# Kernel tuning notes

Hardware: AMD Instinct MI355X
Metric: run time of the kernel (lower is better)

## Reference

```python
import jax, jax.numpy as jnp
import numpy as np

N_NODES = 50000
N_EDGES = 800000
IN_DIM = 128
HID = 32
HEADS = 4
OUT_DIM = 64
NEG_SLOPE = 0.2  # DGL GATConv default


def setup_inputs() -> dict:
    key = jax.random.key(0)
    ks = jax.random.split(key, 20)

    def glorot(k, shape):
        fan = shape[0] + shape[-1]
        return (jax.random.normal(k, shape, jnp.float32) * np.sqrt(2.0 / fan)).astype(jnp.float32)

    inp = {
        "h": jax.random.normal(ks[0], (N_NODES, IN_DIM), jnp.float32),
        "src": jax.random.randint(ks[1], (N_EDGES,), 0, N_NODES, jnp.int32),
        "dst": jax.random.randint(ks[2], (N_EDGES,), 0, N_NODES, jnp.int32),
        # layer 0: in_dim -> hidden, HEADS heads, relu
        "W1": glorot(ks[3], (IN_DIM, HEADS * HID)),
        "al1": glorot(ks[4], (HEADS, HID)),
        "ar1": glorot(ks[5], (HEADS, HID)),
        "b1": jnp.zeros((HEADS * HID,), jnp.float32),
        # layer 1 (hidden): hidden*heads -> hidden, HEADS heads, relu
        "W2": glorot(ks[6], (HEADS * HID, HEADS * HID)),
        "al2": glorot(ks[7], (HEADS, HID)),
        "ar2": glorot(ks[8], (HEADS, HID)),
        "b2": jnp.zeros((HEADS * HID,), jnp.float32),
        # layer 2 (output): hidden*heads -> out_dim, 1 head, no activation
        "W3": glorot(ks[9], (HEADS * HID, OUT_DIM)),
        "al3": glorot(ks[10], (1, OUT_DIM)),
        "ar3": glorot(ks[11], (1, OUT_DIM)),
        "b3": jnp.zeros((OUT_DIM,), jnp.float32),
    }
    return inp


def gat_conv(h, src, dst, W, attn_l, attn_r, bias, heads, out_dim, use_relu):
    n = h.shape[0]
    feat = (h @ W).reshape(n, heads, out_dim)              # [N,H,D]
    el = jnp.sum(feat * attn_l[None], axis=-1)             # [N,H]
    er = jnp.sum(feat * attn_r[None], axis=-1)             # [N,H]
    e = jax.nn.leaky_relu(el[src] + er[dst], NEG_SLOPE)    # [E,H] per-edge logits
    # segment softmax over incoming edges of each dst node
    emax = jax.ops.segment_max(e, dst, num_segments=n)     # [N,H] (-inf for isolated nodes, never gathered)
    ee = jnp.exp(e - emax[dst])                            # [E,H]
    denom = jax.ops.segment_sum(ee, dst, num_segments=n)   # [N,H]
    alpha = ee / denom[dst]                                # [E,H]
    msg = feat[src] * alpha[:, :, None]                    # [E,H,D] gather + weight
    out = jax.ops.segment_sum(msg, dst, num_segments=n)    # [N,H,D] scatter-add
    out = out + bias.reshape(1, heads, out_dim)
    if use_relu:
        out = jax.nn.relu(out)
    return out.reshape(n, heads * out_dim)


def reference(h, src, dst, W1, al1, ar1, b1, W2, al2, ar2, b2, W3, al3, ar3, b3):
    # dropout is identity in eval mode
    h1 = gat_conv(h, src, dst, W1, al1, ar1, b1, HEADS, HID, True)
    h2 = gat_conv(h1, src, dst, W2, al2, ar2, b2, HEADS, HID, True)
    h3 = gat_conv(h2, src, dst, W3, al3, ar3, b3, 1, OUT_DIM, False)
    return h3
```

## Files before the change

kernel.cpp:

```cpp
#include <hip/hip_runtime.h>
#include <hip/hip_fp16.h>

#define NNODES 50000
#define NEDGES 800000
#define HISTB 256

__device__ __forceinline__ float leaky(float x) { return x >= 0.f ? x : 0.2f * x; }

typedef _Float16 f16x8 __attribute__((ext_vector_type(8)));
typedef float f32x4 __attribute__((ext_vector_type(4)));

struct __align__(8)  half4v { __half2 h0, h1; };
struct __align__(16) half8v { __half2 h0, h1, h2, h3; };

template<int F, int H, bool FP16IN, bool DO_HIST>
__global__ __launch_bounds__(256) void gemm_mfma_k(const void* __restrict__ Xv,
                                                   const float* __restrict__ W,
                                                   const float* __restrict__ al,
                                                   const float* __restrict__ ar,
                                                   __half* __restrict__ Yh,
                                                   float* __restrict__ el,
                                                   float* __restrict__ er, int n,
                                                   int nGemm,
                                                   const int* __restrict__ dst,
                                                   int* __restrict__ cnt,
                                                   int* __restrict__ rank) {
    constexpr int K = 128;
    constexpr int ROWS = 64;
    constexpr int LDK = K + 8;
    constexpr int NT = F / 16;

    if (DO_HIST && blockIdx.x >= nGemm) {
        int b = blockIdx.x - nGemm;
        for (int e = b * 256 + threadIdx.x; e < NEDGES; e += HISTB * 256)
            rank[e] = atomicAdd(&cnt[dst[e]], 1);
        return;
    }

    __shared__ __align__(16) __half Xs[ROWS * LDK];
    __shared__ __align__(16) __half Wt[F * LDK];

    const int tid = threadIdx.x;
    const int r0 = blockIdx.x * ROWS;

    if constexpr (FP16IN) {
        const __half* X = (const __half*)Xv;
        for (int i = tid; i < ROWS * (K / 8); i += 256) {
            int r = i >> 4, c8 = i & 15;
            int row = r0 + r;
            half8v v;
            __half2 z = __halves2half2(__float2half_rn(0.f), __float2half_rn(0.f));
            v.h0 = z; v.h1 = z; v.h2 = z; v.h3 = z;
            if (row < n) v = ((const half8v*)X)[(size_t)row * (K / 8) + c8];
            *(half8v*)&Xs[r * LDK + c8 * 8] = v;
        }
    } else {
        const float* X = (const float*)Xv;
        for (int i = tid; i < ROWS * (K / 4); i += 256) {
            int r = i >> 5, c4 = i & 31;
            int row = r0 + r;
            float4 v = (row < n) ? ((const float4*)X)[(size_t)row * (K / 4) + c4]
                                 : make_float4(0.f, 0.f, 0.f, 0.f);
            __half* d = &Xs[r * LDK + c4 * 4];
            d[0] = __float2half_rn(v.x); d[1] = __float2half_rn(v.y);
            d[2] = __float2half_rn(v.z); d[3] = __float2half_rn(v.w);
        }
    }
    for (int i = tid; i < K * (F / 4); i += 256) {
        int k = i / (F / 4), n4 = i % (F / 4);
        float4 v = ((const float4*)W)[i];
        int nn = n4 * 4;
        Wt[(nn + 0) * LDK + k] = __float2half_rn(v.x);
        Wt[(nn + 1) * LDK + k] = __float2half_rn(v.y);
        Wt[(nn + 2) * LDK + k] = __float2half_rn(v.z);
        Wt[(nn + 3) * LDK + k] = __float2half_rn(v.w);
    }
    __syncthreads();

    const int wv = tid >> 6, lane = tid & 63;
    const int cl = lane & 15, kg = lane >> 4;

    f32x4 acc[NT];
    #pragma unroll
    for (int t = 0; t < NT; t++) acc[t] = (f32x4){0.f, 0.f, 0.f, 0.f};

    #pragma unroll
    for (int ks = 0; ks < K / 32; ks++) {
        f16x8 a = *(const f16x8*)&Xs[(16 * wv + cl) * LDK + ks * 32 + kg * 8];
        #pragma unroll
        for (int t = 0; t < NT; t++) {
            f16x8 b = *(const f16x8*)&Wt[(16 * t + cl) * LDK + ks * 32 + kg * 8];
            acc[t] = __builtin_amdgcn_mfma_f32_16x16x32_f16(a, b, acc[t], 0, 0, 0);
        }
    }

    #pragma unroll
    for (int t = 0; t < NT; t++)
        #pragma unroll
        for (int j = 0; j < 4; j++) {
            int row = r0 + 16 * wv + 4 * kg + j;
            if (row < n) Yh[(size_t)row * F + 16 * t + cl] = __float2half_rn(acc[t][j]);
        }

    float alv[NT], arv[NT];
    #pragma unroll
    for (int t = 0; t < NT; t++) { alv[t] = al[16 * t + cl]; arv[t] = ar[16 * t + cl]; }

    if (H == 1) {
        float pl[4], pr[4];
        #pragma unroll
        for (int j = 0; j < 4; j++) {
            pl[j] = 0.f; pr[j] = 0.f;
            #pragma unroll
            for (int t = 0; t < NT; t++) { pl[j] += acc[t][j] * alv[t]; pr[j] += acc[t][j] * arv[t]; }
        }
        #pragma unroll
        for (int off = 1; off < 16; off <<= 1)
            #pragma unroll
            for (int j = 0; j < 4; j++) { pl[j] += __shfl_xor(pl[j], off); pr[j] += __shfl_xor(pr[j], off); }
        if (cl == 0)
            #pragma unroll
            for (int j = 0; j < 4; j++) {
                int row = r0 + 16 * wv + 4 * kg + j;
                if (row < n) { el[row] = pl[j]; er[row] = pr[j]; }
            }
    } else {
        float pl[4][4], pr[4][4];
        #pragma unroll
        for (int hh = 0; hh < 4; hh++)
            #pragma unroll
            for (int j = 0; j < 4; j++) {
                pl[hh][j] = acc[2 * hh][j] * alv[2 * hh] + acc[2 * hh + 1][j] * alv[2 * hh + 1];
                pr[hh][j] = acc[2 * hh][j] * arv[2 * hh] + acc[2 * hh + 1][j] * arv[2 * hh + 1];
            }
        #pragma unroll
        for (int off = 1; off < 16; off <<= 1)
            #pragma unroll
            for (int hh = 0; hh < 4; hh++)
                #pragma unroll
                for (int j = 0; j < 4; j++) {
                    pl[hh][j] += __shfl_xor(pl[hh][j], off);
                    pr[hh][j] += __shfl_xor(pr[hh][j], off);
                }
        if (cl == 0)
            #pragma unroll
            for (int j = 0; j < 4; j++) {
                int row = r0 + 16 * wv + 4 * kg + j;
                if (row < n)
                    #pragma unroll
                    for (int hh = 0; hh < 4; hh++) {
                        el[row * 4 + hh] = pl[hh][j];
                        er[row * 4 + hh] = pr[hh][j];
                    }
            }
    }
}

__global__ void scan_blk_k(const int* __restrict__ cnt, int* __restrict__ offs,
                           int* __restrict__ bsum, int n) {
    __shared__ int sm[256];
    int tid = threadIdx.x;
    int i = blockIdx.x * 256 + tid;
    int v = (i < n) ? cnt[i] : 0;
    sm[tid] = v;
    __syncthreads();
    for (int off = 1; off < 256; off <<= 1) {
        int t = (tid >= off) ? sm[tid - off] : 0;
        __syncthreads();
        sm[tid] += t;
        __syncthreads();
    }
    if (i < n) offs[i] = sm[tid] - v;
    if (tid == 255) bsum[blockIdx.x] = sm[255];
}

__global__ void scan_addtop_k(int* __restrict__ offs, const int* __restrict__ bsum,
                              int n, int nb) {
    __shared__ int sm[256];
    int tid = threadIdx.x;
    int v = (tid < nb) ? bsum[tid] : 0;
    sm[tid] = v;
    __syncthreads();
    for (int off = 1; off < 256; off <<= 1) {
        int t = (tid >= off) ? sm[tid - off] : 0;
        __syncthreads();
        sm[tid] += t;
        __syncthreads();
    }
    int prefix = (blockIdx.x > 0) ? sm[blockIdx.x - 1] : 0;
    int i = blockIdx.x * 256 + tid;
    if (i < n) offs[i] += prefix;
    if (i == 0) offs[n] = NEDGES;
}

__global__ void scatter_k(const int* __restrict__ src, const int* __restrict__ dst,
                          const int* __restrict__ rank, const int* __restrict__ offs,
                          int* __restrict__ esrc) {
    int e = blockIdx.x * blockDim.x + threadIdx.x;
    if (e < NEDGES) esrc[offs[dst[e]] + rank[e]] = src[e];
}

__global__ __launch_bounds__(256) void node_agg4_k(const int* __restrict__ offs,
                                                   const int* __restrict__ esrc,
                                                   const float* __restrict__ el,
                                                   const float* __restrict__ er,
                                                   const __half* __restrict__ feat,
                                                   const float* __restrict__ bias,
                                                   __half* __restrict__ out) {
    const int lane = threadIdx.x & 63;
    const int gw0 = (blockIdx.x * 256 + threadIdx.x) >> 6;
    const int NW = (gridDim.x * 256) >> 6;

    const int h  = lane & 3;
    const int q  = lane >> 4;
    const int cl = lane & 15;
    const int hd = cl >> 2;

    float4 ba = *(const float4*)&bias[8 * cl];
    float4 bb = *(const float4*)&bias[8 * cl + 4];

    for (int wid = gw0; wid < NNODES; wid += NW) {
        int beg = offs[wid], end = offs[wid + 1];
        float erh = er[wid * 4 + h];

        float acc[8] = {0.f, 0.f, 0.f, 0.f, 0.f, 0.f, 0.f, 0.f};
        float dsum = 0.f;
        for (int base = beg; base < end; base += 16) {
            int rem = end - base;
            if (rem > 16) rem = 16;
            int sv = 0;
            if (lane < rem) sv = esrc[base + lane];
            int se = __shfl(sv, lane >> 2);
            float p = 0.f;
            if ((lane >> 2) < rem)
                p = __expf(leaky(el[se * 4 + h] + erh));
            dsum += p;
            #pragma unroll
            for (int e = 0; e < 16 && e < rem; e += 4) {
                int eidx = e + q;
                int s = __shfl(sv, eidx);
                float a = __shfl(p, eidx * 4 + hd);
                half8v hv = *(const half8v*)&feat[(size_t)s * 128 + 8 * cl];
                float2 f0 = __half22float2(hv.h0);
                float2 f1 = __half22float2(hv.h1);
                float2 f2 = __half22float2(hv.h2);
                float2 f3 = __half22float2(hv.h3);
                acc[0] += f0.x * a; acc[1] += f0.y * a;
                acc[2] += f1.x * a; acc[3] += f1.y * a;
                acc[4] += f2.x * a; acc[5] += f2.y * a;
                acc[6] += f3.x * a; acc[7] += f3.y * a;
            }
        }
        #pragma unroll
        for (int c = 0; c < 8; c++) {
            acc[c] += __shfl_xor(acc[c], 16);
            acc[c] += __shfl_xor(acc[c], 32);
        }
        #pragma unroll
        for (int off = 4; off < 64; off <<= 1) dsum += __shfl_xor(dsum, off);
        float dh = __shfl(dsum, hd);
        float inv = dh > 0.f ? 1.f / dh : 0.f;
        if (q == 0) {
            float v0 = fmaxf(acc[0] * inv + ba.x, 0.f), v1 = fmaxf(acc[1] * inv + ba.y, 0.f);
            float v2 = fmaxf(acc[2] * inv + ba.z, 0.f), v3 = fmaxf(acc[3] * inv + ba.w, 0.f);
            float v4 = fmaxf(acc[4] * inv + bb.x, 0.f), v5 = fmaxf(acc[5] * inv + bb.y, 0.f);
            float v6 = fmaxf(acc[6] * inv + bb.z, 0.f), v7 = fmaxf(acc[7] * inv + bb.w, 0.f);
            half8v hv;
            hv.h0 = __halves2half2(__float2half_rn(v0), __float2half_rn(v1));
            hv.h1 = __halves2half2(__float2half_rn(v2), __float2half_rn(v3));
            hv.h2 = __halves2half2(__float2half_rn(v4), __float2half_rn(v5));
            hv.h3 = __halves2half2(__float2half_rn(v6), __float2half_rn(v7));
            *(half8v*)&out[(size_t)wid * 128 + 8 * cl] = hv;
        }
    }
}

__global__ __launch_bounds__(256) void node_agg1_k(const int* __restrict__ offs,
                                                   const int* __restrict__ esrc,
                                                   const float* __restrict__ el,
                                                   const float* __restrict__ er,
                                                   const __half* __restrict__ feat,
                                                   const float* __restrict__ bias,
                                                   float* __restrict__ out) {
    const int lane = threadIdx.x & 63;
    const int gw0 = (blockIdx.x * 256 + threadIdx.x) >> 6;
    const int NW = (gridDim.x * 256) >> 6;

    const int q  = lane >> 4;
    const int cl = lane & 15;
    float4 b4 = *(const float4*)&bias[4 * cl];

    for (int wid = gw0; wid < NNODES; wid += NW) {
        int beg = offs[wid], end = offs[wid + 1];
        float erd = er[wid];

        float acc[4] = {0.f, 0.f, 0.f, 0.f};
        float dsum = 0.f;
        for (int base = beg; base < end; base += 64) {
            int rem = end - base;
            if (rem > 64) rem = 64;
            int sv = 0;
            float p = 0.f;
            if (lane < rem) {
                sv = esrc[base + lane];
                p = __expf(leaky(el[sv] + erd));
            }
            dsum += p;
            #pragma unroll 4
            for (int e = 0; e < rem; e += 4) {
                int eidx = e + q;
                int s = __shfl(sv, eidx);
                float a = __shfl(p, eidx);
                half4v hv = *(const half4v*)&feat[(size_t)s * 64 + 4 * cl];
                float2 f0 = __half22float2(hv.h0);
                float2 f1 = __half22float2(hv.h1);
                acc[0] += f0.x * a; acc[1] += f0.y * a;
                acc[2] += f1.x * a; acc[3] += f1.y * a;
            }
        }
        #pragma unroll
        for (int c = 0; c < 4; c++) {
            acc[c] += __shfl_xor(acc[c], 16);
            acc[c] += __shfl_xor(acc[c], 32);
        }
        #pragma unroll
        for (int off = 1; off < 64; off <<= 1) dsum += __shfl_xor(dsum, off);
        float inv = dsum > 0.f ? 1.f / dsum : 0.f;
        if (q == 0) {
            *(float4*)&out[(size_t)wid * 64 + 4 * cl] =
                make_float4(acc[0] * inv + b4.x, acc[1] * inv + b4.y,
                            acc[2] * inv + b4.z, acc[3] * inv + b4.w);
        }
    }
}

extern "C" void kernel_launch(void* const* d_in, const int* in_sizes, int n_in,
                              void* d_out, int out_size, void* d_ws, size_t ws_size,
                              hipStream_t stream) {
    const float* h   = (const float*)d_in[0];
    const int*   src = (const int*)d_in[1];
    const int*   dst = (const int*)d_in[2];
    const float* W1  = (const float*)d_in[3];
    const float* al1 = (const float*)d_in[4];
    const float* ar1 = (const float*)d_in[5];
    const float* b1  = (const float*)d_in[6];
    const float* W2  = (const float*)d_in[7];
    const float* al2 = (const float*)d_in[8];
    const float* ar2 = (const float*)d_in[9];
    const float* b2  = (const float*)d_in[10];
    const float* W3  = (const float*)d_in[11];
    const float* al3 = (const float*)d_in[12];
    const float* ar3 = (const float*)d_in[13];
    const float* b3  = (const float*)d_in[14];
    float* out = (float*)d_out;

    const int n = NNODES;
    __half* feat16 = (__half*)d_ws;
    __half* hbuf16 = feat16 + (size_t)n * 128;
    float*  el     = (float*)(hbuf16 + (size_t)n * 128);
    float*  er     = el + (size_t)n * 4;
    int*    cnt    = (int*)(er + (size_t)n * 4);
    int*    offs   = cnt + n;
    int*    esrc   = offs + (n + 1);
    int*    bsum   = esrc + NEDGES;
    int*    rank   = bsum + 256;

    const int gemmBlocks = (n + 63) / 64;
    const int nBlk = (n + 255) / 256;
    const int eBlk = (NEDGES + 255) / 256;
    const int aggBlk = 2048;

    hipMemsetAsync(cnt, 0, (size_t)n * sizeof(int), stream);

    gemm_mfma_k<128, 4, false, true><<<gemmBlocks + HISTB, 256, 0, stream>>>(
        h, W1, al1, ar1, feat16, el, er, n, gemmBlocks, dst, cnt, rank);

    scan_blk_k<<<nBlk, 256, 0, stream>>>(cnt, offs, bsum, n);
    scan_addtop_k<<<nBlk, 256, 0, stream>>>(offs, bsum, n, nBlk);
    scatter_k<<<eBlk, 256, 0, stream>>>(src, dst, rank, offs, esrc);

    node_agg4_k<<<aggBlk, 256, 0, stream>>>(offs, esrc, el, er, feat16, b1, hbuf16);

    gemm_mfma_k<128, 4, true, false><<<gemmBlocks, 256, 0, stream>>>(
        hbuf16, W2, al2, ar2, feat16, el, er, n, gemmBlocks, nullptr, nullptr, nullptr);
    node_agg4_k<<<aggBlk, 256, 0, stream>>>(offs, esrc, el, er, feat16, b2, hbuf16);

    gemm_mfma_k<64, 1, true, false><<<gemmBlocks, 256, 0, stream>>>(
        hbuf16, W3, al3, ar3, feat16, el, er, n, gemmBlocks, nullptr, nullptr, nullptr);
    node_agg1_k<<<aggBlk, 256, 0, stream>>>(offs, esrc, el, er, feat16, b3, out);
}
```

Before: 222.1 us.

## Pretranspose weights to fp16 once and load GEMM operands directly from global

A new small kernel converts and transposes all three weight matrices to fp16 once per call into workspace. The GEMM kernels drop their shared-memory staging of X and W and read MFMA operands straight from global memory. Each block no longer converts and transposes the full weight matrix into LDS, and the barrier goes away. The cost is one extra launch, plus weight reads that rely on L2/L1 caching and A-loads that may be less coalesced.

```diff
diff --git a/kernel.cpp b/kernel.cpp
--- a/kernel.cpp
+++ b/kernel.cpp
@@ -13,9 +13,26 @@
 struct __align__(8)  half4v { __half2 h0, h1; };
 struct __align__(16) half8v { __half2 h0, h1, h2, h3; };
 
+__global__ __launch_bounds__(256) void wtrans_k(const float* __restrict__ W1,
+                                                const float* __restrict__ W2,
+                                                const float* __restrict__ W3,
+                                                __half* __restrict__ Wt) {
+    int i = blockIdx.x * 256 + threadIdx.x;
+    if (i < 16384) {
+        int k = i >> 7, c = i & 127;
+        Wt[c * 128 + k] = __float2half_rn(W1[i]);
+    } else if (i < 32768) {
+        int e = i - 16384, k = e >> 7, c = e & 127;
+        Wt[16384 + c * 128 + k] = __float2half_rn(W2[e]);
+    } else if (i < 40960) {
+        int e = i - 32768, k = e >> 6, c = e & 63;
+        Wt[32768 + c * 128 + k] = __float2half_rn(W3[e]);
+    }
+}
+
 template<int F, int H, bool FP16IN, bool DO_HIST>
 __global__ __launch_bounds__(256) void gemm_mfma_k(const void* __restrict__ Xv,
-                                                   const float* __restrict__ W,
+                                                   const __half* __restrict__ Wt,
                                                    const float* __restrict__ al,
                                                    const float* __restrict__ ar,
                                                    __half* __restrict__ Yh,
@@ -26,8 +43,6 @@
                                                    int* __restrict__ cnt,
                                                    int* __restrict__ rank) {
     constexpr int K = 128;
-    constexpr int ROWS = 64;
-    constexpr int LDK = K + 8;
     constexpr int NT = F / 16;
 
     if (DO_HIST && blockIdx.x >= nGemm) {
@@ -37,48 +52,12 @@
         return;
     }
 
-    __shared__ __align__(16) __half Xs[ROWS * LDK];
-    __shared__ __align__(16) __half Wt[F * LDK];
-
     const int tid = threadIdx.x;
-    const int r0 = blockIdx.x * ROWS;
-
-    if constexpr (FP16IN) {
-        const __half* X = (const __half*)Xv;
-        for (int i = tid; i < ROWS * (K / 8); i += 256) {
-            int r = i >> 4, c8 = i & 15;
-            int row = r0 + r;
-            half8v v;
-            __half2 z = __halves2half2(__float2half_rn(0.f), __float2half_rn(0.f));
-            v.h0 = z; v.h1 = z; v.h2 = z; v.h3 = z;
-            if (row < n) v = ((const half8v*)X)[(size_t)row * (K / 8) + c8];
-            *(half8v*)&Xs[r * LDK + c8 * 8] = v;
-        }
-    } else {
-        const float* X = (const float*)Xv;
-        for (int i = tid; i < ROWS * (K / 4); i += 256) {
-            int r = i >> 5, c4 = i & 31;
-            int row = r0 + r;
-            float4 v = (row < n) ? ((const float4*)X)[(size_t)row * (K / 4) + c4]
-                                 : make_float4(0.f, 0.f, 0.f, 0.f);
-            __half* d = &Xs[r * LDK + c4 * 4];
-            d[0] = __float2half_rn(v.x); d[1] = __float2half_rn(v.y);
-            d[2] = __float2half_rn(v.z); d[3] = __float2half_rn(v.w);
-        }
-    }
-    for (int i = tid; i < K * (F / 4); i += 256) {
-        int k = i / (F / 4), n4 = i % (F / 4);
-        float4 v = ((const float4*)W)[i];
-        int nn = n4 * 4;
-        Wt[(nn + 0) * LDK + k] = __float2half_rn(v.x);
-        Wt[(nn + 1) * LDK + k] = __float2half_rn(v.y);
-        Wt[(nn + 2) * LDK + k] = __float2half_rn(v.z);
-        Wt[(nn + 3) * LDK + k] = __float2half_rn(v.w);
-    }
-    __syncthreads();
-
     const int wv = tid >> 6, lane = tid & 63;
     const int cl = lane & 15, kg = lane >> 4;
+    const int r0 = blockIdx.x * 64;
+    const int rowA = r0 + 16 * wv + cl;
+    const int rA = rowA < n ? rowA : n - 1;
 
     f32x4 acc[NT];
     #pragma unroll
@@ -86,10 +65,21 @@
 
     #pragma unroll
     for (int ks = 0; ks < K / 32; ks++) {
-        f16x8 a = *(const f16x8*)&Xs[(16 * wv + cl) * LDK + ks * 32 + kg * 8];
+        f16x8 a;
+        if constexpr (FP16IN) {
+            a = *(const f16x8*)((const __half*)Xv + (size_t)rA * K + ks * 32 + kg * 8);
+        } else {
+            const float* Xp = (const float*)Xv + (size_t)rA * K + ks * 32 + kg * 8;
+            float4 x0 = *(const float4*)Xp;
+            float4 x1 = *(const float4*)(Xp + 4);
+            a[0] = (_Float16)x0.x; a[1] = (_Float16)x0.y;
+            a[2] = (_Float16)x0.z; a[3] = (_Float16)x0.w;
+            a[4] = (_Float16)x1.x; a[5] = (_Float16)x1.y;
+            a[6] = (_Float16)x1.z; a[7] = (_Float16)x1.w;
+        }
         #pragma unroll
         for (int t = 0; t < NT; t++) {
-            f16x8 b = *(const f16x8*)&Wt[(16 * t + cl) * LDK + ks * 32 + kg * 8];
+            f16x8 b = *(const f16x8*)(Wt + (size_t)(16 * t + cl) * K + ks * 32 + kg * 8);
             acc[t] = __builtin_amdgcn_mfma_f32_16x16x32_f16(a, b, acc[t], 0, 0, 0);
         }
     }
@@ -364,6 +354,8 @@
     int*    esrc   = offs + (n + 1);
     int*    bsum   = esrc + NEDGES;
     int*    rank   = bsum + 256;
+    __half* wt     = (__half*)(rank + NEDGES);
+    __half* wt1 = wt, *wt2 = wt + 16384, *wt3 = wt + 32768;
 
     const int gemmBlocks = (n + 63) / 64;
     const int nBlk = (n + 255) / 256;
@@ -371,9 +363,10 @@
     const int aggBlk = 2048;
 
     hipMemsetAsync(cnt, 0, (size_t)n * sizeof(int), stream);
+    wtrans_k<<<160, 256, 0, stream>>>(W1, W2, W3, wt);
 
     gemm_mfma_k<128, 4, false, true><<<gemmBlocks + HISTB, 256, 0, stream>>>(
-        h, W1, al1, ar1, feat16, el, er, n, gemmBlocks, dst, cnt, rank);
+        h, wt1, al1, ar1, feat16, el, er, n, gemmBlocks, dst, cnt, rank);
 
     scan_blk_k<<<nBlk, 256, 0, stream>>>(cnt, offs, bsum, n);
     scan_addtop_k<<<nBlk, 256, 0, stream>>>(offs, bsum, n, nBlk);
@@ -382,10 +375,10 @@
     node_agg4_k<<<aggBlk, 256, 0, stream>>>(offs, esrc, el, er, feat16, b1, hbuf16);
 
     gemm_mfma_k<128, 4, true, false><<<gemmBlocks, 256, 0, stream>>>(
-        hbuf16, W2, al2, ar2, feat16, el, er, n, gemmBlocks, nullptr, nullptr, nullptr);
+        hbuf16, wt2, al2, ar2, feat16, el, er, n, gemmBlocks, nullptr, nullptr, nullptr);
     node_agg4_k<<<aggBlk, 256, 0, stream>>>(offs, esrc, el, er, feat16, b2, hbuf16);
 
     gemm_mfma_k<64, 1, true, false><<<gemmBlocks, 256, 0, stream>>>(
-        hbuf16, W3, al3, ar3, feat16, el, er, n, gemmBlocks, nullptr, nullptr, nullptr);
+        hbuf16, wt3, al3, ar3, feat16, el, er, n, gemmBlocks, nullptr, nullptr, nullptr);
     node_agg1_k<<<aggBlk, 256, 0, stream>>>(offs, esrc, el, er, feat16, b3, out);
 }
```

Result: no change. 221.1 us (-0.4%).
